# Performance work log

Measured on AMD Instinct MI355X. Metric: run time of the kernel, lower is better.

## Reference

```python
import jax, jax.numpy as jnp
import numpy as np

EPS = 1e-5


def setup_inputs() -> dict:
    key = jax.random.key(0)
    x = jax.random.normal(key, (16, 128, 513), dtype=jnp.float32)
    return {"x": x}


def reference(x):
    N, C, T = x.shape
    # split into even / odd time indices
    x1 = x[:, :, 0::2]                      # (N, C, t) with t = ceil(T/2)
    x2 = x[:, :, 1::2]                      # (N, C, p) with p = floor(T/2)
    # outer-product score: exp(x1)[...,t] * exp(-x2)[...,p]  -> (N, C, t, p)
    g = jnp.exp(x1)[:, :, :, None] * jnp.exp(-x2)[:, :, None, :]
    g = jnp.log(g + EPS) ** 2
    # mean over channels, then exp -> (N, t, p)
    RAM = jnp.exp(jnp.sum(g, axis=1) / C)
    # normalizeRAM: threshold + sum-based symmetric normalization
    RAM = jnp.where(RAM < 0.5, jnp.zeros_like(RAM), RAM)
    da = jnp.sum(RAM, axis=1)               # (N, p)  sum over t
    db = jnp.sum(RAM, axis=2)               # (N, t)  sum over p
    norm = (db[:, :, None] * da[:, None, :] + EPS) ** -0.5
    RAM = RAM * norm                         # (N, t, p)
    # upsample by 2 along both dims, drop last row -> (N, T, T-1)
    RAM = jnp.repeat(RAM, 2, axis=1)[:, :-1, :]
    RAM = jnp.repeat(RAM, 2, axis=2)
    # einsum 'nct,ntp->nct' == x * sum_p RAM
    return x * jnp.sum(RAM, axis=2)[:, None, :]
```

## Files before the change

### kernel.cpp

```cpp
#include <hip/hip_runtime.h>
#include <math.h>

#define N_B 16
#define C_CH 128
#define T_LEN 513
#define NI 257
#define NJ 256
#define SCALE (1.4426950408889634f/128.0f)

typedef unsigned u32;
typedef unsigned short u16;
typedef short bf16x8 __attribute__((ext_vector_type(8)));
typedef float f32x4 __attribute__((ext_vector_type(4)));

#define RAM_F 0
#define PDA_F (N_B*NI*NJ)

__device__ inline u32 cvtpk(float a, float b) {
    u32 r;
    asm("v_cvt_pk_bf16_f32 %0, %1, %2" : "=v"(r) : "v"(a), "v"(b));
    return r;
}

__device__ inline void cvt8(const float* fa, bf16x8& hv, bf16x8& lv) {
    union { u32 w[4]; bf16x8 v; } H, L;
    #pragma unroll
    for (int p = 0; p < 4; ++p) {
        const float a = fa[2*p], b = fa[2*p+1];
        const u32 h = cvtpk(a, b);
        const float la = a - __builtin_bit_cast(float, h << 16);
        const float lb = b - __builtin_bit_cast(float, h & 0xffff0000u);
        H.w[p] = h;
        L.w[p] = cvtpk(la, lb);
    }
    hv = H.v; lv = L.v;
}

__global__ __launch_bounds__(512, 4) void k1(const float* __restrict__ x,
                                             float* __restrict__ ram,
                                             float* __restrict__ pda) {
    __shared__ float As[32][132];
    __shared__ float Bs[64][132];
    const int jq = blockIdx.x, ib = blockIdx.y, n = blockIdx.z;
    const int i0 = ib * 32, j0 = jq * 64;
    const int tid = threadIdx.x;
    const int l = tid & 63, wv = tid >> 6;
    const float* xn = x + (size_t)n * (C_CH * T_LEN);
    float* rn = ram + (size_t)n * NI * NJ;

    {
        const int e = l & 31, chalf = l >> 5;
        #pragma unroll
        for (int m = 0; m < 8; ++m) {
            const int c = wv * 16 + 2 * m + chalf;
            const int idx = c * T_LEN + 2 * i0 + 2 * e;
            const float2 f2 = *(const float2*)(xn + (idx & ~1));
            As[e][c] = (idx & 1) ? f2.y : f2.x;
        }
        #pragma unroll
        for (int m = 0; m < 16; ++m) {
            const int c = wv * 16 + m;
            const int idx = c * T_LEN + 2 * j0 + 2 * l + 1;
            const float2 f2 = *(const float2*)(xn + (idx & ~1));
            Bs[l][c] = (idx & 1) ? f2.y : f2.x;
        }
    }
    __syncthreads();

    const int il = l & 15, g = l >> 4;
    const int ih = wv >> 2, jt = wv & 3;
    {
        bf16x8 ah[4], al[4], bh[4], bl[4];
        float psum = 0.f, qsq = 0.f;
        #pragma unroll
        for (int kc = 0; kc < 4; ++kc) {
            float fa[8], fb[8];
            const float* ap = &As[ih * 16 + il][kc * 32 + 8 * g];
            const float* bp = &Bs[jt * 16 + il][kc * 32 + 8 * g];
            #pragma unroll
            for (int e = 0; e < 8; ++e) { fa[e] = ap[e]; fb[e] = bp[e]; }
            #pragma unroll
            for (int e = 0; e < 8; ++e) {
                psum = fmaf(fa[e], fa[e], psum);
                qsq  = fmaf(fb[e], fb[e], qsq);
            }
            cvt8(fa, ah[kc], al[kc]);
            cvt8(fb, bh[kc], bl[kc]);
        }
        psum += __shfl_xor(psum, 16, 64);
        psum += __shfl_xor(psum, 32, 64);
        qsq  += __shfl_xor(qsq, 16, 64);
        qsq  += __shfl_xor(qsq, 32, 64);
        float pv[4];
        #pragma unroll
        for (int r = 0; r < 4; ++r) pv[r] = __shfl(psum, 4 * g + r, 64);

        f32x4 acc = {0.f, 0.f, 0.f, 0.f};
        #pragma unroll
        for (int kc = 0; kc < 4; ++kc) {
            acc = __builtin_amdgcn_mfma_f32_16x16x32_bf16(ah[kc], bh[kc], acc, 0, 0, 0);
            acc = __builtin_amdgcn_mfma_f32_16x16x32_bf16(ah[kc], bl[kc], acc, 0, 0, 0);
            acc = __builtin_amdgcn_mfma_f32_16x16x32_bf16(al[kc], bh[kc], acc, 0, 0, 0);
        }
        const int j = j0 + jt * 16 + il;
        float cs = 0.f;
        #pragma unroll
        for (int r = 0; r < 4; ++r) {
            const int i = i0 + ih * 16 + 4 * g + r;
            const float rv = exp2f((pv[r] + qsq - 2.f * acc[r]) * SCALE);
            rn[(size_t)i * NJ + j] = rv;
            cs += rv;
        }
        cs += __shfl_xor(cs, 16, 64);
        cs += __shfl_xor(cs, 32, 64);
        if (l < 16) pda[((size_t)n * 17 + ib * 2 + ih) * NJ + j0 + jt * 16 + l] = cs;
    }

    if (ib == 0) {
        const int jl = tid >> 3, sub = tid & 7;
        float sab = 0.f, saa = 0.f, sbb = 0.f;
        #pragma unroll
        for (int e = 0; e < 16; ++e) {
            const int c = sub * 16 + e;
            const float a = xn[c * T_LEN + 512];
            const float b = Bs[jl][c];
            sab = fmaf(a, b, sab);
            saa = fmaf(a, a, saa);
            sbb = fmaf(b, b, sbb);
        }
        #pragma unroll
        for (int o = 4; o; o >>= 1) {
            sab += __shfl_xor(sab, o, 64);
            saa += __shfl_xor(saa, o, 64);
            sbb += __shfl_xor(sbb, o, 64);
        }
        if (sub == 0) {
            const float rv = exp2f((saa + sbb - 2.f * sab) * SCALE);
            rn[(size_t)256 * NJ + j0 + jl] = rv;
            pda[((size_t)n * 17 + 16) * NJ + j0 + jl] = rv;
        }
    }
}

__global__ __launch_bounds__(256) void k2(const float* __restrict__ ram,
                                          const float* __restrict__ pda,
                                          const float* __restrict__ x,
                                          float* __restrict__ out) {
    const int ic = blockIdx.x, n = blockIdx.y;
    __shared__ float w_s[NJ];
    __shared__ float f_s[16];
    const int tid = threadIdx.x;
    {
        float da = 0.f;
        #pragma unroll
        for (int k = 0; k < 17; ++k) da += pda[((size_t)n * 17 + k) * NJ + tid];
        w_s[tid] = rsqrtf(da);
    }
    __syncthreads();
    const int wv = tid >> 6, lane = tid & 63;
    #pragma unroll
    for (int rr = 0; rr < 4; ++rr) {
        const int lr = wv * 4 + rr;
        const int i = ic * 16 + lr;
        if (i < NI) {
            const float* rrow = ram + ((size_t)n * NI + i) * NJ;
            float db = 0.f, t0 = 0.f;
            #pragma unroll
            for (int k = 0; k < 4; ++k) {
                const float v = rrow[lane + 64 * k];
                db += v;
                t0 = fmaf(v, w_s[lane + 64 * k], t0);
            }
            #pragma unroll
            for (int off = 32; off; off >>= 1) {
                db += __shfl_xor(db, off, 64);
                t0 += __shfl_xor(t0, off, 64);
            }
            if (lane == 0) f_s[lr] = 2.f * t0 * rsqrtf(db);
        }
    }
    __syncthreads();
    const int tt = tid & 31, cgp = tid >> 5;
    const int t = ic * 32 + tt;
    if (t < T_LEN) {
        const float f = f_s[tt >> 1];
        const float* xn = x + (size_t)n * C_CH * T_LEN;
        float* on = out + (size_t)n * C_CH * T_LEN;
        #pragma unroll
        for (int p = 0; p < 16; ++p) {
            const int c = cgp * 16 + p;
            on[c * T_LEN + t] = xn[c * T_LEN + t] * f;
        }
    }
}

extern "C" void kernel_launch(void* const* d_in, const int* in_sizes, int n_in,
                              void* d_out, int out_size, void* d_ws, size_t ws_size,
                              hipStream_t stream) {
    const float* x = (const float*)d_in[0];
    float* out = (float*)d_out;
    float* ws = (float*)d_ws;
    float* ram = ws + RAM_F;
    float* pda = ws + PDA_F;

    k1<<<dim3(4, 8, N_B), 512, 0, stream>>>(x, ram, pda);
    k2<<<dim3(17, N_B), 256, 0, stream>>>(ram, pda, x, out);
}
```

Baseline: 21.44 us.

## Enlarge k1 tile to 64x64 so each wave computes two MFMA row blocks

The i-tile of the pairwise-distance kernel grows from 32 to 64 rows, so each of the 8 waves now holds two 16-row A fragments and reuses its B fragment across both MFMA chains. This halves the grid (4x4x16 blocks) and the partial column-sum rows (17 to 9). It aims to cut redundant B loads and bf16 splitting per output and reduce per-block overhead. In exchange it doubles LDS for A, lowers the occupancy hint to 2, and launches fewer blocks (256), which may underfill the GPU.

```diff
diff --git a/kernel.cpp b/kernel.cpp
--- a/kernel.cpp
+++ b/kernel.cpp
@@ -6,6 +6,7 @@
 #define T_LEN 513
 #define NI 257
 #define NJ 256
+#define NPD 9
 #define SCALE (1.4426950408889634f/128.0f)
 
 typedef unsigned u32;
@@ -36,84 +37,101 @@
     hv = H.v; lv = L.v;
 }
 
-__global__ __launch_bounds__(512, 4) void k1(const float* __restrict__ x,
+__global__ __launch_bounds__(512, 2) void k1(const float* __restrict__ x,
                                              float* __restrict__ ram,
                                              float* __restrict__ pda) {
-    __shared__ float As[32][132];
+    __shared__ float As[64][132];
     __shared__ float Bs[64][132];
-    const int jq = blockIdx.x, ib = blockIdx.y, n = blockIdx.z;
-    const int i0 = ib * 32, j0 = jq * 64;
+    const int jb = blockIdx.x, ib = blockIdx.y, n = blockIdx.z;
+    const int i0 = ib * 64, j0 = jb * 64;
     const int tid = threadIdx.x;
     const int l = tid & 63, wv = tid >> 6;
     const float* xn = x + (size_t)n * (C_CH * T_LEN);
     float* rn = ram + (size_t)n * NI * NJ;
 
     {
-        const int e = l & 31, chalf = l >> 5;
-        #pragma unroll
-        for (int m = 0; m < 8; ++m) {
-            const int c = wv * 16 + 2 * m + chalf;
-            const int idx = c * T_LEN + 2 * i0 + 2 * e;
-            const float2 f2 = *(const float2*)(xn + (idx & ~1));
-            As[e][c] = (idx & 1) ? f2.y : f2.x;
-        }
         #pragma unroll
         for (int m = 0; m < 16; ++m) {
             const int c = wv * 16 + m;
-            const int idx = c * T_LEN + 2 * j0 + 2 * l + 1;
-            const float2 f2 = *(const float2*)(xn + (idx & ~1));
-            Bs[l][c] = (idx & 1) ? f2.y : f2.x;
+            {
+                const int idx = c * T_LEN + 2 * i0 + 2 * l;
+                const float2 f2 = *(const float2*)(xn + (idx & ~1));
+                As[l][c] = (idx & 1) ? f2.y : f2.x;
+            }
+            {
+                const int idx = c * T_LEN + 2 * j0 + 2 * l + 1;
+                const float2 f2 = *(const float2*)(xn + (idx & ~1));
+                Bs[l][c] = (idx & 1) ? f2.y : f2.x;
+            }
         }
     }
     __syncthreads();
 
     const int il = l & 15, g = l >> 4;
-    const int ih = wv >> 2, jt = wv & 3;
+    const int ia = wv >> 2, jt = wv & 3;
     {
-        bf16x8 ah[4], al[4], bh[4], bl[4];
-        float psum = 0.f, qsq = 0.f;
+        bf16x8 ah[2][4], al[2][4], bh[4], bl[4];
+        float psum[2] = {0.f, 0.f}, qsq = 0.f;
         #pragma unroll
         for (int kc = 0; kc < 4; ++kc) {
-            float fa[8], fb[8];
-            const float* ap = &As[ih * 16 + il][kc * 32 + 8 * g];
+            float fb[8];
             const float* bp = &Bs[jt * 16 + il][kc * 32 + 8 * g];
             #pragma unroll
-            for (int e = 0; e < 8; ++e) { fa[e] = ap[e]; fb[e] = bp[e]; }
-            #pragma unroll
-            for (int e = 0; e < 8; ++e) {
-                psum = fmaf(fa[e], fa[e], psum);
-                qsq  = fmaf(fb[e], fb[e], qsq);
-            }
-            cvt8(fa, ah[kc], al[kc]);
+            for (int e = 0; e < 8; ++e) fb[e] = bp[e];
+            #pragma unroll
+            for (int e = 0; e < 8; ++e) qsq = fmaf(fb[e], fb[e], qsq);
             cvt8(fb, bh[kc], bl[kc]);
-        }
-        psum += __shfl_xor(psum, 16, 64);
-        psum += __shfl_xor(psum, 32, 64);
-        qsq  += __shfl_xor(qsq, 16, 64);
-        qsq  += __shfl_xor(qsq, 32, 64);
-        float pv[4];
-        #pragma unroll
-        for (int r = 0; r < 4; ++r) pv[r] = __shfl(psum, 4 * g + r, 64);
-
-        f32x4 acc = {0.f, 0.f, 0.f, 0.f};
+            #pragma unroll
+            for (int s = 0; s < 2; ++s) {
+                float fa[8];
+                const float* ap = &As[ia * 32 + s * 16 + il][kc * 32 + 8 * g];
+                #pragma unroll
+                for (int e = 0; e < 8; ++e) fa[e] = ap[e];
+                #pragma unroll
+                for (int e = 0; e < 8; ++e) psum[s] = fmaf(fa[e], fa[e], psum[s]);
+                cvt8(fa, ah[s][kc], al[s][kc]);
+            }
+        }
+        #pragma unroll
+        for (int s = 0; s < 2; ++s) {
+            psum[s] += __shfl_xor(psum[s], 16, 64);
+            psum[s] += __shfl_xor(psum[s], 32, 64);
+        }
+        qsq += __shfl_xor(qsq, 16, 64);
+        qsq += __shfl_xor(qsq, 32, 64);
+        float pv[2][4];
+        #pragma unroll
+        for (int s = 0; s < 2; ++s)
+            #pragma unroll
+            for (int r = 0; r < 4; ++r) pv[s][r] = __shfl(psum[s], 4 * g + r, 64);
+
+        f32x4 acc[2];
+        acc[0] = (f32x4){0.f, 0.f, 0.f, 0.f};
+        acc[1] = (f32x4){0.f, 0.f, 0.f, 0.f};
         #pragma unroll
         for (int kc = 0; kc < 4; ++kc) {
-            acc = __builtin_amdgcn_mfma_f32_16x16x32_bf16(ah[kc], bh[kc], acc, 0, 0, 0);
-            acc = __builtin_amdgcn_mfma_f32_16x16x32_bf16(ah[kc], bl[kc], acc, 0, 0, 0);
-            acc = __builtin_amdgcn_mfma_f32_16x16x32_bf16(al[kc], bh[kc], acc, 0, 0, 0);
+            #pragma unroll
+            for (int s = 0; s < 2; ++s) {
+                acc[s] = __builtin_amdgcn_mfma_f32_16x16x32_bf16(ah[s][kc], bh[kc], acc[s], 0, 0, 0);
+                acc[s] = __builtin_amdgcn_mfma_f32_16x16x32_bf16(ah[s][kc], bl[kc], acc[s], 0, 0, 0);
+                acc[s] = __builtin_amdgcn_mfma_f32_16x16x32_bf16(al[s][kc], bh[kc], acc[s], 0, 0, 0);
+            }
         }
         const int j = j0 + jt * 16 + il;
         float cs = 0.f;
         #pragma unroll
-        for (int r = 0; r < 4; ++r) {
-            const int i = i0 + ih * 16 + 4 * g + r;
-            const float rv = exp2f((pv[r] + qsq - 2.f * acc[r]) * SCALE);
-            rn[(size_t)i * NJ + j] = rv;
-            cs += rv;
+        for (int s = 0; s < 2; ++s) {
+            #pragma unroll
+            for (int r = 0; r < 4; ++r) {
+                const int i = i0 + ia * 32 + s * 16 + 4 * g + r;
+                const float rv = exp2f((pv[s][r] + qsq - 2.f * acc[s][r]) * SCALE);
+                rn[(size_t)i * NJ + j] = rv;
+                cs += rv;
+            }
         }
         cs += __shfl_xor(cs, 16, 64);
         cs += __shfl_xor(cs, 32, 64);
-        if (l < 16) pda[((size_t)n * 17 + ib * 2 + ih) * NJ + j0 + jt * 16 + l] = cs;
+        if (l < 16) pda[((size_t)n * NPD + ib * 2 + ia) * NJ + j0 + jt * 16 + l] = cs;
     }
 
     if (ib == 0) {
@@ -137,7 +155,7 @@
         if (sub == 0) {
             const float rv = exp2f((saa + sbb - 2.f * sab) * SCALE);
             rn[(size_t)256 * NJ + j0 + jl] = rv;
-            pda[((size_t)n * 17 + 16) * NJ + j0 + jl] = rv;
+            pda[((size_t)n * NPD + 8) * NJ + j0 + jl] = rv;
         }
     }
 }
@@ -153,7 +171,7 @@
     {
         float da = 0.f;
         #pragma unroll
-        for (int k = 0; k < 17; ++k) da += pda[((size_t)n * 17 + k) * NJ + tid];
+        for (int k = 0; k < NPD; ++k) da += pda[((size_t)n * NPD + k) * NJ + tid];
         w_s[tid] = rsqrtf(da);
     }
     __syncthreads();
@@ -203,6 +221,6 @@
     float* ram = ws + RAM_F;
     float* pda = ws + PDA_F;
 
-    k1<<<dim3(4, 8, N_B), 512, 0, stream>>>(x, ram, pda);
+    k1<<<dim3(4, 4, N_B), 512, 0, stream>>>(x, ram, pda);
     k2<<<dim3(17, N_B), 256, 0, stream>>>(ram, pda, x, out);
 }
```

Result: faster. 19.35 us (-9.8%).
